# Kernel optimization log

Measured on AMD Instinct MI355X. Metric: run time of the kernel, lower is better.

## Reference

```python
import jax, jax.numpy as jnp
import numpy as np

N_NODES = 50000
N_EDGES = 800000
NUM_L0 = 3
H_CHANNELS = 32
NODE_INV_DIM = NUM_L0 * H_CHANNELS  # 96
H_DIM = 128  # edge_channels_list[0]
IN_DIM = H_DIM + 2 * NODE_INV_DIM  # 320
LN_EPS = 1e-5


def setup_inputs() -> dict:
    key = jax.random.key(0)
    ks = jax.random.split(key, 8)
    node_invariant = jax.random.normal(ks[0], (N_NODES, NODE_INV_DIM), dtype=jnp.float32)
    edge_features = jax.random.normal(ks[1], (N_EDGES, H_DIM), dtype=jnp.float32)
    edge_index = jax.random.randint(ks[2], (2, N_EDGES), 0, N_NODES, dtype=jnp.int32)
    # MLP params (scaled like torch default init ~ 1/sqrt(fan_in))
    W1 = jax.random.normal(ks[3], (IN_DIM, H_DIM), dtype=jnp.float32) / np.sqrt(IN_DIM)
    b1 = jnp.zeros((H_DIM,), dtype=jnp.float32)
    W2 = jax.random.normal(ks[4], (H_DIM, H_DIM), dtype=jnp.float32) / np.sqrt(H_DIM)
    b2 = jnp.zeros((H_DIM,), dtype=jnp.float32)
    ln_gamma = jnp.ones((H_DIM,), dtype=jnp.float32)
    ln_beta = jnp.zeros((H_DIM,), dtype=jnp.float32)
    return {
        "node_invariant": node_invariant,
        "edge_features": edge_features,
        "edge_index": edge_index,
        "W1": W1, "b1": b1, "W2": W2, "b2": b2,
        "ln_gamma": ln_gamma, "ln_beta": ln_beta,
    }


def reference(node_invariant, edge_features, edge_index, W1, b1, W2, b2, ln_gamma, ln_beta):
    # expand_edge: gather per-edge source/destination node invariant (l=0) features
    src = node_invariant[edge_index[0]]   # [E, NODE_INV_DIM]
    dst = node_invariant[edge_index[1]]   # [E, NODE_INV_DIM]
    x = jnp.concatenate([src, dst, edge_features], axis=-1)  # [E, IN_DIM]
    # ff: Linear -> ReLU -> Linear
    h = jax.nn.relu(x @ W1 + b1) @ W2 + b2  # [E, H_DIM]
    # LayerNorm over last dim
    mu = jnp.mean(h, axis=-1, keepdims=True)
    var = jnp.mean(jnp.square(h - mu), axis=-1, keepdims=True)
    hn = (h - mu) * jax.lax.rsqrt(var + LN_EPS) * ln_gamma + ln_beta
    # residual edge update
    return edge_features + hn
```

## Files before the change

kernel.cpp:

```cpp
#include <hip/hip_runtime.h>
#include <stdint.h>

#define N_H    128
#define N_INV  96
#define HS     132
#define EPSF   134
#define TILES  2
#define NWAVE  8
#define CHUNK  256
#define NBLK   256
#define KS1    10
#define KS2    4
#define W1_BYTES 81920
#define W2_BYTES 32768
#define W_BYTES  (W1_BYTES + W2_BYTES)
#define WBUF     4352
#define BIAS_OFF (W_BYTES + NWAVE * WBUF)
#define SMEM_BYTES (BIAS_OFF + 2048)

typedef __bf16 bf16x8 __attribute__((ext_vector_type(8)));
typedef float  f32x4  __attribute__((ext_vector_type(4)));

__device__ __forceinline__ unsigned short f2bf(float f) {
    union { float f; unsigned u; } v; v.f = f;
    unsigned u = v.u;
    u += 0x7FFFu + ((u >> 16) & 1u);
    return (unsigned short)(u >> 16);
}

__global__ void prep_weights(const float* __restrict__ W1,
                             const float* __restrict__ W2,
                             unsigned short* __restrict__ w1p,
                             unsigned short* __restrict__ w2p) {
    int idx = blockIdx.x * blockDim.x + threadIdx.x;
    if (idx < KS1 * 8 * 64 * 8) {
        int j = idx & 7, lane = (idx >> 3) & 63, nt = (idx >> 9) & 7, ks = idx >> 12;
        int k = ks * 32 + (lane >> 4) * 8 + j;
        int n = nt * 16 + (lane & 15);
        w1p[idx] = f2bf(W1[(size_t)k * N_H + n]);
    } else {
        int r = idx - KS1 * 8 * 64 * 8;
        if (r < KS2 * 8 * 64 * 8) {
            int j = r & 7, lane = (r >> 3) & 63, nt = (r >> 9) & 7, ks = r >> 12;
            int k = ks * 32 + (lane >> 4) * 8 + j;
            int n = nt * 16 + (lane & 15);
            w2p[r] = f2bf(W2[(size_t)k * N_H + n]);
        }
    }
}

__global__ void prep_ninv(const float* __restrict__ ninv,
                          unsigned short* __restrict__ nb, int n4) {
    int i = blockIdx.x * blockDim.x + threadIdx.x;
    if (i < n4) {
        float4 v = ((const float4*)ninv)[i];
        ((ushort4*)nb)[i] = make_ushort4(f2bf(v.x), f2bf(v.y), f2bf(v.z), f2bf(v.w));
    }
}

__global__ __launch_bounds__(512, 2)
void edge_mlp(const unsigned short* __restrict__ ninvb, const float* __restrict__ ef,
              const int* __restrict__ ei,
              const unsigned short* __restrict__ wpk,
              const float* __restrict__ b1g, const float* __restrict__ b2g,
              const float* __restrict__ gg, const float* __restrict__ btg,
              float* __restrict__ out, int E, int cbase, int crem) {
    extern __shared__ __align__(16) char smem[];

    const int tid  = threadIdx.x;
    const int wv   = tid >> 6;
    const int lane = tid & 63;
    const int lr   = lane & 15;
    const int lkg  = lane >> 4;
    const int lk   = lkg * 8;
    const int qr   = lkg * 4;

    const int b     = blockIdx.x;
    const int c0    = b * cbase + (b < crem ? b : crem);
    const int cnt   = cbase + (b < crem ? 1 : 0);
    if (cnt <= 0) return;
    const int clast = c0 + cnt - 1;

    {
        const char* gsrc = (const char*)wpk;
        #pragma unroll
        for (int i = 0; i < 14; ++i) {
            int ch = wv * 14 + i;
            __builtin_amdgcn_global_load_lds(
                (const __attribute__((address_space(1))) void*)(gsrc + ch * 1024 + lane * 16),
                (__attribute__((address_space(3))) void*)(smem + ch * 1024),
                16, 0, 0);
        }
        if (wv == 0) {
            const float* srcs[4] = { b1g, b2g, gg, btg };
            #pragma unroll
            for (int a = 0; a < 4; ++a) {
                #pragma unroll
                for (int h = 0; h < 2; ++h) {
                    __builtin_amdgcn_global_load_lds(
                        (const __attribute__((address_space(1))) void*)(srcs[a] + h * 64 + lane),
                        (__attribute__((address_space(3))) void*)(smem + BIAS_OFF + a * 512 + h * 256),
                        4, 0, 0);
                }
            }
        }
    }

    const float* b1l = (const float*)(smem + BIAS_OFF);
    const float* b2l = (const float*)(smem + BIAS_OFF + 512);
    const float* gl  = (const float*)(smem + BIAS_OFF + 1024);
    const float* btl = (const float*)(smem + BIAS_OFF + 1536);

    bf16x8 an[TILES][6];
    f32x4  efa[TILES][4][2];
    int sA[TILES], dA[TILES], eS[TILES], eD[TILES];
    {
        #pragma unroll
        for (int t = 0; t < TILES; ++t) {
            int er = c0 * CHUNK + wv * 32 + t * 16 + lr;
            int ee = er < E ? er : E - 1;
            int s0 = ei[ee], d0 = ei[(size_t)E + ee];
            #pragma unroll
            for (int q = 0; q < 6; ++q) {
                int row = q < 3 ? s0 : d0;
                an[t][q] = *(const bf16x8*)(ninvb + (size_t)row * N_INV + (q % 3) * 32 + lk);
            }
            const float* ap = ef + (size_t)ee * N_H;
            #pragma unroll
            for (int j = 0; j < 4; ++j) {
                efa[t][j][0] = *(const f32x4*)(ap + j * 32 + lk);
                efa[t][j][1] = *(const f32x4*)(ap + j * 32 + lk + 4);
            }
        }
        int c1 = c0 + 1 <= clast ? c0 + 1 : clast;
        #pragma unroll
        for (int t = 0; t < TILES; ++t) {
            int er = c1 * CHUNK + wv * 32 + t * 16 + lr;
            int ee = er < E ? er : E - 1;
            sA[t] = ei[ee]; dA[t] = ei[(size_t)E + ee];
        }
        int c2 = c0 + 2 <= clast ? c0 + 2 : clast;
        #pragma unroll
        for (int t = 0; t < TILES; ++t) {
            int er = c2 * CHUNK + wv * 32 + t * 16 + lr;
            int ee = er < E ? er : E - 1;
            eS[t] = ei[ee]; eD[t] = ei[(size_t)E + ee];
        }
    }

    __syncthreads();

    char* buf = smem + W_BYTES + wv * WBUF;
    unsigned short* hb = (unsigned short*)buf;
    float* ep = (float*)buf;

    for (int c = c0; c <= clast; ++c) {
        f32x4 acc[TILES][8] = {};
        #pragma unroll
        for (int ks = 0; ks < KS1; ++ks) {
            bf16x8 bfr[8];
            #pragma unroll
            for (int nt = 0; nt < 8; ++nt)
                bfr[nt] = *(const bf16x8*)(smem + ((ks * 8 + nt) << 10) + (lane << 4));
            #pragma unroll
            for (int t = 0; t < TILES; ++t) {
                bf16x8 a;
                if (ks < 6) {
                    a = an[t][ks];
                } else {
                    const int j = ks - 6;
                    union { unsigned short us[8]; bf16x8 b; } ua;
                    ua.us[0] = f2bf(efa[t][j][0][0]); ua.us[1] = f2bf(efa[t][j][0][1]);
                    ua.us[2] = f2bf(efa[t][j][0][2]); ua.us[3] = f2bf(efa[t][j][0][3]);
                    ua.us[4] = f2bf(efa[t][j][1][0]); ua.us[5] = f2bf(efa[t][j][1][1]);
                    ua.us[6] = f2bf(efa[t][j][1][2]); ua.us[7] = f2bf(efa[t][j][1][3]);
                    a = ua.b;
                }
                #pragma unroll
                for (int nt = 0; nt < 8; ++nt)
                    acc[t][nt] = __builtin_amdgcn_mfma_f32_16x16x32_bf16(a, bfr[nt], acc[t][nt], 0, 0, 0);
            }
        }

        const int eb = c * CHUNK + wv * 32;

        #pragma unroll
        for (int t = 0; t < TILES; ++t) {
            #pragma unroll
            for (int nt = 0; nt < 8; ++nt) {
                float bb = b1l[nt * 16 + lr];
                #pragma unroll
                for (int i = 0; i < 4; ++i) {
                    float v = acc[t][nt][i] + bb;
                    v = v > 0.0f ? v : 0.0f;
                    hb[(qr + i) * HS + nt * 16 + lr] = f2bf(v);
                }
            }
            __builtin_amdgcn_wave_barrier();

            f32x4 res[2][4];
            #pragma unroll
            for (int h = 0; h < 2; ++h) {
                #pragma unroll
                for (int it = 0; it < 4; ++it) {
                    int cid = it * 64 + lane;
                    int row = cid >> 5, c4 = (cid & 31) << 2;
                    int erow = eb + t * 16 + 8 * h + row;
                    int ec = erow < E ? erow : E - 1;
                    res[h][it] = *(const f32x4*)(ef + (size_t)ec * N_H + c4);
                }
            }

            f32x4 acc2[8] = {};
            #pragma unroll
            for (int ks = 0; ks < KS2; ++ks) {
                bf16x8 a = *(const bf16x8*)((const char*)hb + lr * (HS * 2) + ks * 64 + lkg * 16);
                #pragma unroll
                for (int nt = 0; nt < 8; ++nt) {
                    bf16x8 w = *(const bf16x8*)(smem + W1_BYTES + ((ks * 8 + nt) << 10) + (lane << 4));
                    acc2[nt] = __builtin_amdgcn_mfma_f32_16x16x32_bf16(a, w, acc2[nt], 0, 0, 0);
                }
            }

            if (t == 0) {
                #pragma unroll
                for (int tt = 0; tt < TILES; ++tt) {
                    #pragma unroll
                    for (int q = 0; q < 6; ++q) {
                        int row = q < 3 ? sA[tt] : dA[tt];
                        an[tt][q] = *(const bf16x8*)(ninvb + (size_t)row * N_INV + (q % 3) * 32 + lk);
                    }
                }
                sA[0] = eS[0]; sA[1] = eS[1]; dA[0] = eD[0]; dA[1] = eD[1];
                int c3 = c + 3 <= clast ? c + 3 : clast;
                #pragma unroll
                for (int tt = 0; tt < TILES; ++tt) {
                    int er = c3 * CHUNK + wv * 32 + tt * 16 + lr;
                    int ee = er < E ? er : E - 1;
                    eS[tt] = ei[ee]; eD[tt] = ei[(size_t)E + ee];
                }
            }

            float vals[8][4];
            float s1[4] = {0.f, 0.f, 0.f, 0.f};
            float s2[4] = {0.f, 0.f, 0.f, 0.f};
            #pragma unroll
            for (int nt = 0; nt < 8; ++nt) {
                float bb = b2l[nt * 16 + lr];
                #pragma unroll
                for (int i = 0; i < 4; ++i) {
                    float v = acc2[nt][i] + bb;
                    vals[nt][i] = v;
                    s1[i] += v;
                    s2[i] += v * v;
                }
            }
            #pragma unroll
            for (int m = 1; m < 16; m <<= 1) {
                #pragma unroll
                for (int i = 0; i < 4; ++i) {
                    s1[i] += __shfl_xor(s1[i], m);
                    s2[i] += __shfl_xor(s2[i], m);
                }
            }
            float mu[4], rs[4];
            #pragma unroll
            for (int i = 0; i < 4; ++i) {
                mu[i] = s1[i] * (1.0f / 128.0f);
                float var = s2[i] * (1.0f / 128.0f) - mu[i] * mu[i];
                rs[i] = rsqrtf(var + 1e-5f);
            }

            #pragma unroll
            for (int h = 0; h < 2; ++h) {
                if ((lkg >> 1) == h) {
                    #pragma unroll
                    for (int nt = 0; nt < 8; ++nt) {
                        int cc = nt * 16 + lr;
                        float g  = gl[cc];
                        float bt = btl[cc];
                        #pragma unroll
                        for (int i = 0; i < 4; ++i)
                            ep[(qr - 8 * h + i) * EPSF + cc] = (vals[nt][i] - mu[i]) * rs[i] * g + bt;
                    }
                }
                __builtin_amdgcn_wave_barrier();
                #pragma unroll
                for (int it = 0; it < 4; ++it) {
                    int cid = it * 64 + lane;
                    int row = cid >> 5, c4 = (cid & 31) << 2;
                    int erow = eb + t * 16 + 8 * h + row;
                    if (erow < E) {
                        f32x4 nv = *(const f32x4*)(ep + row * EPSF + c4);
                        *(f32x4*)(out + (size_t)erow * N_H + c4) = nv + res[h][it];
                    }
                }
                __builtin_amdgcn_wave_barrier();
            }
        }

        {
            int cn = c + 1 <= clast ? c + 1 : clast;
            #pragma unroll
            for (int t = 0; t < TILES; ++t) {
                int er = cn * CHUNK + wv * 32 + t * 16 + lr;
                int ee = er < E ? er : E - 1;
                const float* ap = ef + (size_t)ee * N_H;
                #pragma unroll
                for (int j = 0; j < 4; ++j) {
                    efa[t][j][0] = *(const f32x4*)(ap + j * 32 + lk);
                    efa[t][j][1] = *(const f32x4*)(ap + j * 32 + lk + 4);
                }
            }
        }
    }
}

extern "C" void kernel_launch(void* const* d_in, const int* in_sizes, int n_in,
                              void* d_out, int out_size, void* d_ws, size_t ws_size,
                              hipStream_t stream) {
    const float* ninv = (const float*)d_in[0];
    const float* ef   = (const float*)d_in[1];
    const int*   ei   = (const int*)d_in[2];
    const float* W1   = (const float*)d_in[3];
    const float* b1   = (const float*)d_in[4];
    const float* W2   = (const float*)d_in[5];
    const float* b2   = (const float*)d_in[6];
    const float* g    = (const float*)d_in[7];
    const float* bt   = (const float*)d_in[8];
    float* out = (float*)d_out;

    const int E = in_sizes[1] / N_H;
    const int NNODE = in_sizes[0] / N_INV;

    unsigned short* w1p = (unsigned short*)d_ws;
    unsigned short* w2p = w1p + KS1 * 8 * 64 * 8;
    unsigned short* nb  = w2p + KS2 * 8 * 64 * 8;

    hipFuncSetAttribute((const void*)edge_mlp,
                        hipFuncAttributeMaxDynamicSharedMemorySize, SMEM_BYTES);

    int prep_total = (KS1 + KS2) * 8 * 64 * 8;
    prep_weights<<<(prep_total + 255) / 256, 256, 0, stream>>>(W1, W2, w1p, w2p);

    int n4 = NNODE * N_INV / 4;
    prep_ninv<<<(n4 + 255) / 256, 256, 0, stream>>>(ninv, nb, n4);

    int nchunks = (E + CHUNK - 1) / CHUNK;
    int cbase = nchunks / NBLK;
    int crem  = nchunks - cbase * NBLK;
    edge_mlp<<<NBLK, 512, SMEM_BYTES, stream>>>(nb, ef, ei, w1p, b1, b2, g, bt,
                                                out, E, cbase, crem);
}
```

Before: 261.6 us.

## Hoist residual loads and bf16 conversion before GEMM1, add MFMA priority hints

```diff
diff --git a/kernel.cpp b/kernel.cpp
--- a/kernel.cpp
+++ b/kernel.cpp
@@ -151,54 +151,30 @@
     __syncthreads();
 
     char* buf = smem + W_BYTES + wv * WBUF;
-    unsigned short* hb = (unsigned short*)buf;
+    __bf16* hb = (__bf16*)buf;
     float* ep = (float*)buf;
 
     for (int c = c0; c <= clast; ++c) {
-        f32x4 acc[TILES][8] = {};
-        #pragma unroll
-        for (int ks = 0; ks < KS1; ++ks) {
-            bf16x8 bfr[8];
-            #pragma unroll
-            for (int nt = 0; nt < 8; ++nt)
-                bfr[nt] = *(const bf16x8*)(smem + ((ks * 8 + nt) << 10) + (lane << 4));
-            #pragma unroll
-            for (int t = 0; t < TILES; ++t) {
-                bf16x8 a;
-                if (ks < 6) {
-                    a = an[t][ks];
-                } else {
-                    const int j = ks - 6;
-                    union { unsigned short us[8]; bf16x8 b; } ua;
-                    ua.us[0] = f2bf(efa[t][j][0][0]); ua.us[1] = f2bf(efa[t][j][0][1]);
-                    ua.us[2] = f2bf(efa[t][j][0][2]); ua.us[3] = f2bf(efa[t][j][0][3]);
-                    ua.us[4] = f2bf(efa[t][j][1][0]); ua.us[5] = f2bf(efa[t][j][1][1]);
-                    ua.us[6] = f2bf(efa[t][j][1][2]); ua.us[7] = f2bf(efa[t][j][1][3]);
-                    a = ua.b;
-                }
-                #pragma unroll
-                for (int nt = 0; nt < 8; ++nt)
-                    acc[t][nt] = __builtin_amdgcn_mfma_f32_16x16x32_bf16(a, bfr[nt], acc[t][nt], 0, 0, 0);
-            }
-        }
-
         const int eb = c * CHUNK + wv * 32;
 
-        #pragma unroll
-        for (int t = 0; t < TILES; ++t) {
-            #pragma unroll
-            for (int nt = 0; nt < 8; ++nt) {
-                float bb = b1l[nt * 16 + lr];
-                #pragma unroll
-                for (int i = 0; i < 4; ++i) {
-                    float v = acc[t][nt][i] + bb;
-                    v = v > 0.0f ? v : 0.0f;
-                    hb[(qr + i) * HS + nt * 16 + lr] = f2bf(v);
-                }
-            }
-            __builtin_amdgcn_wave_barrier();
-
-            f32x4 res[2][4];
+        bf16x8 anef[TILES][4];
+        #pragma unroll
+        for (int t = 0; t < TILES; ++t) {
+            #pragma unroll
+            for (int j = 0; j < 4; ++j) {
+                union { __bf16 e[8]; bf16x8 v; } u;
+                #pragma unroll
+                for (int m = 0; m < 4; ++m) {
+                    u.e[m]     = (__bf16)efa[t][j][0][m];
+                    u.e[4 + m] = (__bf16)efa[t][j][1][m];
+                }
+                anef[t][j] = u.v;
+            }
+        }
+
+        f32x4 res[TILES][2][4];
+        #pragma unroll
+        for (int t = 0; t < TILES; ++t) {
             #pragma unroll
             for (int h = 0; h < 2; ++h) {
                 #pragma unroll
@@ -207,19 +183,54 @@
                     int row = cid >> 5, c4 = (cid & 31) << 2;
                     int erow = eb + t * 16 + 8 * h + row;
                     int ec = erow < E ? erow : E - 1;
-                    res[h][it] = *(const f32x4*)(ef + (size_t)ec * N_H + c4);
-                }
-            }
+                    res[t][h][it] = *(const f32x4*)(ef + (size_t)ec * N_H + c4);
+                }
+            }
+        }
+
+        f32x4 acc[TILES][8] = {};
+        #pragma unroll
+        for (int ks = 0; ks < KS1; ++ks) {
+            bf16x8 bfr[8];
+            #pragma unroll
+            for (int nt = 0; nt < 8; ++nt)
+                bfr[nt] = *(const bf16x8*)(smem + ((ks * 8 + nt) << 10) + (lane << 4));
+            #pragma unroll
+            for (int t = 0; t < TILES; ++t) {
+                bf16x8 a = (ks < 6) ? an[t][ks] : anef[t][ks - 6];
+                __builtin_amdgcn_s_setprio(1);
+                #pragma unroll
+                for (int nt = 0; nt < 8; ++nt)
+                    acc[t][nt] = __builtin_amdgcn_mfma_f32_16x16x32_bf16(a, bfr[nt], acc[t][nt], 0, 0, 0);
+                __builtin_amdgcn_s_setprio(0);
+            }
+        }
+
+        #pragma unroll
+        for (int t = 0; t < TILES; ++t) {
+            #pragma unroll
+            for (int nt = 0; nt < 8; ++nt) {
+                float bb = b1l[nt * 16 + lr];
+                #pragma unroll
+                for (int i = 0; i < 4; ++i) {
+                    float v = acc[t][nt][i] + bb;
+                    v = v > 0.0f ? v : 0.0f;
+                    hb[(qr + i) * HS + nt * 16 + lr] = (__bf16)v;
+                }
+            }
+            __builtin_amdgcn_wave_barrier();
 
             f32x4 acc2[8] = {};
             #pragma unroll
             for (int ks = 0; ks < KS2; ++ks) {
                 bf16x8 a = *(const bf16x8*)((const char*)hb + lr * (HS * 2) + ks * 64 + lkg * 16);
+                __builtin_amdgcn_s_setprio(1);
                 #pragma unroll
                 for (int nt = 0; nt < 8; ++nt) {
                     bf16x8 w = *(const bf16x8*)(smem + W1_BYTES + ((ks * 8 + nt) << 10) + (lane << 4));
                     acc2[nt] = __builtin_amdgcn_mfma_f32_16x16x32_bf16(a, w, acc2[nt], 0, 0, 0);
                 }
+                __builtin_amdgcn_s_setprio(0);
             }
 
             if (t == 0) {
@@ -292,7 +303,7 @@
                     int erow = eb + t * 16 + 8 * h + row;
                     if (erow < E) {
                         f32x4 nv = *(const f32x4*)(ep + row * EPSF + c4);
-                        *(f32x4*)(out + (size_t)erow * N_H + c4) = nv + res[h][it];
+                        *(f32x4*)(out + (size_t)erow * N_H + c4) = nv + res[t][h][it];
                     }
                 }
                 __builtin_amdgcn_wave_barrier();
```

Measured after the change: 374.2 us. 43.0% more time.
